# Optimization experiments

Hardware: AMD Instinct MI355X
Metric: run time of the kernel (lower is better)

## Reference

```python
import jax, jax.numpy as jnp
import numpy as np

VOCAB, EMB, HID = 50000, 256, 512
H = HID // 2            # per-direction LSTM hidden
NTAGS, START, STOP = 16, 14, 15
T = 2048                # sequence length
NEG = -10000.0


def setup_inputs() -> dict:
    key = jax.random.key(0)
    ks = jax.random.split(key, 13)
    s = 0.1  # param scale
    trans = jax.random.normal(ks[10], (NTAGS, NTAGS), jnp.float32)
    trans = trans.at[START, :].set(NEG).at[:, STOP].set(NEG)
    return {
        "sentence": jax.random.randint(ks[0], (T,), 0, VOCAB),
        "embed":  jax.random.normal(ks[1], (VOCAB, EMB), jnp.float32) * s,
        "w_ih_f": jax.random.normal(ks[2], (4 * H, EMB), jnp.float32) * s,
        "w_hh_f": jax.random.normal(ks[3], (4 * H, H), jnp.float32) * s,
        "b_f":    jax.random.normal(ks[4], (4 * H,), jnp.float32) * s,
        "w_ih_b": jax.random.normal(ks[5], (4 * H, EMB), jnp.float32) * s,
        "w_hh_b": jax.random.normal(ks[6], (4 * H, H), jnp.float32) * s,
        "b_b":    jax.random.normal(ks[7], (4 * H,), jnp.float32) * s,
        "w_out":  jax.random.normal(ks[8], (NTAGS, HID), jnp.float32) * s,
        "b_out":  jax.random.normal(ks[9], (NTAGS,), jnp.float32) * s,
        "transitions": trans,
        "h0": jax.random.normal(ks[11], (2, H), jnp.float32),
        "c0": jax.random.normal(ks[12], (2, H), jnp.float32),
    }


def _lstm_scan(xs, h0, c0, w_ih, w_hh, b):
    # xs: [T, EMB]; PyTorch gate order i, f, g, o
    def step(carry, x):
        h, c = carry
        g = x @ w_ih.T + h @ w_hh.T + b            # [4H]
        i, f, gg, o = jnp.split(g, 4)
        c = jax.nn.sigmoid(f) * c + jax.nn.sigmoid(i) * jnp.tanh(gg)
        h = jax.nn.sigmoid(o) * jnp.tanh(c)
        return (h, c), h
    _, hs = jax.lax.scan(step, (h0, c0), xs)
    return hs                                      # [T, H]


def _features(sentence, embed, w_ih_f, w_hh_f, b_f, w_ih_b, w_hh_b, b_b,
              w_out, b_out, h0, c0):
    xs = embed[sentence]                           # [T, EMB]
    hf = _lstm_scan(xs, h0[0], c0[0], w_ih_f, w_hh_f, b_f)
    hb = jnp.flip(_lstm_scan(jnp.flip(xs, 0), h0[1], c0[1], w_ih_b, w_hh_b, b_b), 0)
    lstm_out = jnp.concatenate([hf, hb], axis=-1)  # [T, HID]
    return lstm_out @ w_out.T + b_out              # [T, NTAGS]


def _viterbi(feats, transitions):
    init = jnp.full((NTAGS,), NEG, feats.dtype).at[START].set(0.0)

    def step(fv, feat):
        m = fv[None, :] + transitions              # [next, prev]
        return jnp.max(m, axis=1) + feat, jnp.argmax(m, axis=1)
    fv, bps = jax.lax.scan(step, init, feats)
    term = fv + transitions[STOP]
    best = jnp.argmax(term)
    score = term[best]

    def back(tag, bp):
        nt = bp[tag]
        return nt, nt
    _, ys = jax.lax.scan(back, best, jnp.flip(bps, 0))
    # [best, tag_{T-2}, ..., tag_0, START] -> drop START, reverse
    path = jnp.flip(jnp.concatenate([best[None], ys])[:-1])
    return score, path


def reference(sentence, embed, w_ih_f, w_hh_f, b_f, w_ih_b, w_hh_b, b_b,
              w_out, b_out, transitions, h0, c0):
    feats = _features(sentence, embed, w_ih_f, w_hh_f, b_f,
                      w_ih_b, w_hh_b, b_b, w_out, b_out, h0, c0)
    score, tag_seq = _viterbi(feats, transitions)
    return score, tag_seq
```

## Files before the change

### kernel.cpp

```cpp
#include <hip/hip_runtime.h>

typedef unsigned int u32;
typedef u32 u32x8 __attribute__((ext_vector_type(8)));

#define TT 2048
#define HD 256
#define G4 1024
#define NT 16
#define START_TAG 14
#define STOP_TAG 15
#define NEGV (-10000.0f)

__device__ __forceinline__ int sdot4e(u32 a, u32 b, int c) {
#if __has_builtin(__builtin_amdgcn_sdot4)
    return __builtin_amdgcn_sdot4((int)a, (int)b, c, false);
#else
    c += (int)(signed char)(a & 255) * (int)(signed char)(b & 255);
    c += (int)(signed char)((a >> 8) & 255) * (int)(signed char)((b >> 8) & 255);
    c += (int)(signed char)((a >> 16) & 255) * (int)(signed char)((b >> 16) & 255);
    c += (int)(signed char)(a >> 24) * (int)(signed char)(b >> 24);
    return c;
#endif
}
__device__ __forceinline__ float sigmf_(float x) { return 1.0f / (1.0f + __expf(-x)); }
__device__ __forceinline__ float tanhf_(float x) {
    float e = __expf(-2.0f * fabsf(x));
    return copysignf((1.0f - e) / (1.0f + e), x);
}

__global__ __launch_bounds__(256) void pack_q8(const float* whh_f, const float* whh_b,
                                               u32* wreg8, float* rowscale) {
    int lane = threadIdx.x & 63;
    int row = blockIdx.x * 4 + (threadIdx.x >> 6);
    int dir = row >> 10, r = row & 1023;
    const float* w = (dir ? whh_b : whh_f) + (size_t)r * HD + lane * 4;
    float4 v = *((const float4*)w);
    float m = fmaxf(fmaxf(fabsf(v.x), fabsf(v.y)), fmaxf(fabsf(v.z), fabsf(v.w)));
    for (int off = 1; off < 64; off <<= 1) m = fmaxf(m, __shfl_xor(m, off, 64));
    float invs = m > 0.f ? 127.f / m : 0.f;
    int q0 = (int)rintf(v.x * invs), q1 = (int)rintf(v.y * invs);
    int q2 = (int)rintf(v.z * invs), q3 = (int)rintf(v.w * invs);
    u32 pk = (u32)(q0 & 255) | ((u32)(q1 & 255) << 8) |
             ((u32)(q2 & 255) << 16) | ((u32)(q3 & 255) << 24);
    wreg8[((size_t)(dir * 1024 + r)) * 64 + lane] = pk;
    if (lane == 0) rowscale[dir * 1024 + r] = m * (1.0f / (127.f * 64.f));
}

__global__ __launch_bounds__(256) void input_gemm(const int* sent, const float* embed,
                                                  const float* wih_f, const float* b_f,
                                                  const float* wih_b, const float* b_b,
                                                  float* G) {
    __shared__ float X[16][HD];
    __shared__ int rows[16];
    int tid = threadIdx.x;
    int dir = blockIdx.z;
    int t0 = blockIdx.x * 16;
    if (tid < 16) {
        int tg = t0 + tid;
        rows[tid] = sent[dir ? (TT - 1 - tg) : tg];
    }
    __syncthreads();
    for (int i = 0; i < 16; i++) X[i][tid] = embed[(size_t)rows[i] * HD + tid];
    __syncthreads();
    int r = blockIdx.y * 256 + tid;
    const float* wrow = (dir ? wih_b : wih_f) + (size_t)r * HD;
    float acc[16];
#pragma unroll
    for (int i = 0; i < 16; i++) acc[i] = 0.0f;
    for (int kc = 0; kc < HD / 4; kc++) {
        float4 w4 = ((const float4*)wrow)[kc];
#pragma unroll
        for (int i = 0; i < 16; i++) {
            float4 x4 = *((const float4*)&X[i][kc * 4]);
            acc[i] += w4.x * x4.x + w4.y * x4.y + w4.z * x4.z + w4.w * x4.w;
        }
    }
    float bias = (dir ? b_b : b_f)[r];
    for (int i = 0; i < 16; i++)
        G[((size_t)dir * TT + t0 + i) * G4 + r] = acc[i] + bias;
}

#define DOTQ2(W0, W1, HB)                                                     \
    {                                                                         \
        uint4 pa = *((const uint4*)&h2q[(HB)]);                               \
        acc0 = sdot4e(W0[0], pa.x, acc0); acc1 = sdot4e(W1[0], pa.x, acc1);   \
        acc0 = sdot4e(W0[1], pa.y, acc0); acc1 = sdot4e(W1[1], pa.y, acc1);   \
        acc0 = sdot4e(W0[2], pa.z, acc0); acc1 = sdot4e(W1[2], pa.z, acc1);   \
        acc0 = sdot4e(W0[3], pa.w, acc0); acc1 = sdot4e(W1[3], pa.w, acc1);   \
        uint4 pb = *((const uint4*)&h2q[(HB) + 4]);                           \
        acc0 = sdot4e(W0[4], pb.x, acc0); acc1 = sdot4e(W1[4], pb.x, acc1);   \
        acc0 = sdot4e(W0[5], pb.y, acc0); acc1 = sdot4e(W1[5], pb.y, acc1);   \
        acc0 = sdot4e(W0[6], pb.z, acc0); acc1 = sdot4e(W1[6], pb.z, acc1);   \
        acc0 = sdot4e(W0[7], pb.w, acc0); acc1 = sdot4e(W1[7], pb.w, acc1);   \
    }

__global__ __launch_bounds__(512, 1)
void lstm_rec(const u32* wreg8, const float* rowscale,
              const float* G, const float* h0, const float* c0, float* H) {
    __shared__ float fo[2][256];
    __shared__ __align__(16) u32 h2q[64];
    int tid = threadIdx.x;
    int dir = blockIdx.x;
    const u32x8* p0 = (const u32x8*)(wreg8 + ((size_t)dir * 1024 + tid) * 64);
    const u32x8* p1 = (const u32x8*)(wreg8 + ((size_t)dir * 1024 + tid + 512) * 64);
    u32x8 wq00 = p0[0], wq01 = p0[1], wq02 = p0[2], wq03 = p0[3],
          wq04 = p0[4], wq05 = p0[5], wq06 = p0[6], wq07 = p0[7];
    u32x8 wq10 = p1[0], wq11 = p1[1], wq12 = p1[2], wq13 = p1[3],
          wq14 = p1[4], wq15 = p1[5], wq16 = p1[6], wq17 = p1[7];
    float cr0 = rowscale[dir * 1024 + tid];
    float cr1 = rowscale[dir * 1024 + tid + 512];
    float cst = 0.0f;
    if (tid < 256) {
        cst = c0[dir * HD + tid];
        float hv = h0[dir * HD + tid];
        hv = fminf(fmaxf(hv, -1.984375f), 1.984375f);
        ((signed char*)h2q)[tid] = (signed char)(int)rintf(hv * 64.f);
    }
    __syncthreads();
    const float* Gd = G + (size_t)dir * TT * G4;
    float* Hd = H + (size_t)dir * TT * HD;
    for (int t = 0; t < TT; t++) {
        float g0 = Gd[(size_t)t * G4 + tid];
        float g1 = Gd[(size_t)t * G4 + tid + 512];
        int acc0 = 0, acc1 = 0;
        DOTQ2(wq00, wq10, 0)  DOTQ2(wq01, wq11, 8)
        DOTQ2(wq02, wq12, 16) DOTQ2(wq03, wq13, 24)
        DOTQ2(wq04, wq14, 32) DOTQ2(wq05, wq15, 40)
        DOTQ2(wq06, wq16, 48) DOTQ2(wq07, wq17, 56)
        float e0 = (float)acc0 * cr0 + g0;
        float e1 = (float)acc1 * cr1 + g1;
        float x0, x1;
        if (tid >= 256) {
            fo[0][tid - 256] = sigmf_(e0);
            fo[1][tid - 256] = sigmf_(e1);
        } else {
            x0 = sigmf_(e0);
            x1 = tanhf_(e1);
        }
        __syncthreads();
        if (tid < 256) {
            float sf = fo[0][tid], so = fo[1][tid];
            cst = sf * cst + x0 * x1;
            float h = so * tanhf_(cst);
            Hd[(size_t)t * HD + tid] = h;
            ((signed char*)h2q)[tid] = (signed char)(int)rintf(h * 64.f);
        }
        __syncthreads();
    }
}

__global__ __launch_bounds__(256) void feats_kernel(const float* H, const float* w_out,
                                                    const float* b_out, float* feats) {
    int idx = blockIdx.x * blockDim.x + threadIdx.x;
    int t = idx >> 4, n = idx & 15;
    const float* hf = H + (size_t)t * HD;
    const float* hb = H + ((size_t)TT + (TT - 1 - t)) * HD;
    const float* w = w_out + (size_t)n * (2 * HD);
    float a = b_out[n];
    for (int k = 0; k < HD; k += 4) {
        float4 h4 = *((const float4*)&hf[k]);
        float4 w4 = *((const float4*)&w[k]);
        a += h4.x * w4.x + h4.y * w4.y + h4.z * w4.z + h4.w * w4.w;
    }
    for (int k = 0; k < HD; k += 4) {
        float4 h4 = *((const float4*)&hb[k]);
        float4 w4 = *((const float4*)&w[HD + k]);
        a += h4.x * w4.x + h4.y * w4.y + h4.z * w4.z + h4.w * w4.w;
    }
    feats[(size_t)t * NT + n] = a;
}

__global__ __launch_bounds__(64) void viterbi_kernel(const float* feats, const float* trans,
                                                     float* out) {
    __shared__ float fl[4096];
    __shared__ float fvs[NT];
    __shared__ unsigned char bps[TT][NT];
    int lane = threadIdx.x;
    int n = lane >> 2, pg = lane & 3;
    float4 tr4 = *((const float4*)&trans[n * NT + pg * 4]);
    float vft = (n == START_TAG) ? 0.0f : NEGV;
    for (int c = 0; c < TT / 256; c++) {
        float4 st[16];
        const float4* src = (const float4*)(feats + c * 4096);
#pragma unroll
        for (int i = 0; i < 16; i++) st[i] = src[i * 64 + lane];
#pragma unroll
        for (int i = 0; i < 16; i++) *((float4*)&fl[(i * 64 + lane) * 4]) = st[i];
        __syncthreads();
        for (int tt = 0; tt < 256; tt++) {
            int t = c * 256 + tt;
            float f0 = __shfl(vft, ((pg << 2) + 0) << 2, 64);
            float f1 = __shfl(vft, ((pg << 2) + 1) << 2, 64);
            float f2 = __shfl(vft, ((pg << 2) + 2) << 2, 64);
            float f3 = __shfl(vft, ((pg << 2) + 3) << 2, 64);
            float ft = fl[tt * 16 + n];
            float v = f0 + tr4.x; int bi = pg * 4 + 0;
            float v1 = f1 + tr4.y; if (v1 > v) { v = v1; bi = pg * 4 + 1; }
            float v2 = f2 + tr4.z; if (v2 > v) { v = v2; bi = pg * 4 + 2; }
            float v3 = f3 + tr4.w; if (v3 > v) { v = v3; bi = pg * 4 + 3; }
#pragma unroll
            for (int m = 1; m <= 2; m <<= 1) {
                float ov = __shfl_xor(v, m, 64);
                int ob = __shfl_xor(bi, m, 64);
                if (ov > v || (ov == v && ob < bi)) { v = ov; bi = ob; }
            }
            if (pg == 0) bps[t][n] = (unsigned char)bi;
            vft = v + ft;
        }
        __syncthreads();
    }
    if ((lane & 3) == 0) fvs[n] = vft;
    __syncthreads();
    if (lane == 0) {
        float best = -3.0e38f; int bt = 0;
        for (int p = 0; p < NT; p++) {
            float tv = fvs[p] + trans[STOP_TAG * NT + p];
            if (tv > best) { best = tv; bt = p; }
        }
        out[0] = best;
        int tag = bt;
        out[TT] = (float)tag;
        for (int t = TT - 2; t >= 0; t--) {
            tag = bps[t + 1][tag];
            out[1 + t] = (float)tag;
        }
    }
}

extern "C" void kernel_launch(void* const* d_in, const int* in_sizes, int n_in,
                              void* d_out, int out_size, void* d_ws, size_t ws_size,
                              hipStream_t stream) {
    const int* sent = (const int*)d_in[0];
    const float* embed = (const float*)d_in[1];
    const float* wih_f = (const float*)d_in[2];
    const float* whh_f = (const float*)d_in[3];
    const float* b_f = (const float*)d_in[4];
    const float* wih_b = (const float*)d_in[5];
    const float* whh_b = (const float*)d_in[6];
    const float* b_b = (const float*)d_in[7];
    const float* w_out = (const float*)d_in[8];
    const float* b_out = (const float*)d_in[9];
    const float* trans = (const float*)d_in[10];
    const float* h0 = (const float*)d_in[11];
    const float* c0 = (const float*)d_in[12];
    float* out = (float*)d_out;
    char* ws = (char*)d_ws;

    float* G = (float*)(ws);
    float* H = (float*)(ws + (size_t)16 * 1024 * 1024);
    float* feats = (float*)(ws + (size_t)20 * 1024 * 1024);
    u32* wreg8 = (u32*)(ws + (size_t)21 * 1024 * 1024);
    float* rowscale = (float*)(ws + (size_t)22 * 1024 * 1024);

    pack_q8<<<dim3(512), 256, 0, stream>>>(whh_f, whh_b, wreg8, rowscale);
    input_gemm<<<dim3(TT / 16, G4 / 256, 2), 256, 0, stream>>>(sent, embed, wih_f, b_f,
                                                               wih_b, b_b, G);
    lstm_rec<<<dim3(2), 512, 0, stream>>>(wreg8, rowscale, G, h0, c0, H);
    feats_kernel<<<dim3(TT * NT / 256), 256, 0, stream>>>(H, w_out, b_out, feats);
    viterbi_kernel<<<dim3(1), 64, 0, stream>>>(feats, trans, out);
}
```

Before: 2.610 ms.

## Drop one barrier per LSTM step and parallelize Viterbi backtrace

```diff
diff --git a/kernel.cpp b/kernel.cpp
--- a/kernel.cpp
+++ b/kernel.cpp
@@ -82,12 +82,12 @@
 
 #define DOTQ2(W0, W1, HB)                                                     \
     {                                                                         \
-        uint4 pa = *((const uint4*)&h2q[(HB)]);                               \
+        uint4 pa = *((const uint4*)&hbp[(HB)]);                               \
         acc0 = sdot4e(W0[0], pa.x, acc0); acc1 = sdot4e(W1[0], pa.x, acc1);   \
         acc0 = sdot4e(W0[1], pa.y, acc0); acc1 = sdot4e(W1[1], pa.y, acc1);   \
         acc0 = sdot4e(W0[2], pa.z, acc0); acc1 = sdot4e(W1[2], pa.z, acc1);   \
         acc0 = sdot4e(W0[3], pa.w, acc0); acc1 = sdot4e(W1[3], pa.w, acc1);   \
-        uint4 pb = *((const uint4*)&h2q[(HB) + 4]);                           \
+        uint4 pb = *((const uint4*)&hbp[(HB) + 4]);                           \
         acc0 = sdot4e(W0[4], pb.x, acc0); acc1 = sdot4e(W1[4], pb.x, acc1);   \
         acc0 = sdot4e(W0[5], pb.y, acc0); acc1 = sdot4e(W1[5], pb.y, acc1);   \
         acc0 = sdot4e(W0[6], pb.z, acc0); acc1 = sdot4e(W1[6], pb.z, acc1);   \
@@ -97,31 +97,42 @@
 __global__ __launch_bounds__(512, 1)
 void lstm_rec(const u32* wreg8, const float* rowscale,
               const float* G, const float* h0, const float* c0, float* H) {
-    __shared__ float fo[2][256];
-    __shared__ __align__(16) u32 h2q[64];
+    __shared__ __align__(16) u32 h2q[2][64];
     int tid = threadIdx.x;
+    int lane = tid & 63;
+    int wv = tid >> 6;
+    int lo = lane & 31;
+    int half = lane >> 5;
+    int e = wv * 32 + lo;
+    int row0 = half * 256 + e;
+    int row1 = row0 + 512;
     int dir = blockIdx.x;
-    const u32x8* p0 = (const u32x8*)(wreg8 + ((size_t)dir * 1024 + tid) * 64);
-    const u32x8* p1 = (const u32x8*)(wreg8 + ((size_t)dir * 1024 + tid + 512) * 64);
+    const u32x8* p0 = (const u32x8*)(wreg8 + ((size_t)dir * 1024 + row0) * 64);
+    const u32x8* p1 = (const u32x8*)(wreg8 + ((size_t)dir * 1024 + row1) * 64);
     u32x8 wq00 = p0[0], wq01 = p0[1], wq02 = p0[2], wq03 = p0[3],
           wq04 = p0[4], wq05 = p0[5], wq06 = p0[6], wq07 = p0[7];
     u32x8 wq10 = p1[0], wq11 = p1[1], wq12 = p1[2], wq13 = p1[3],
           wq14 = p1[4], wq15 = p1[5], wq16 = p1[6], wq17 = p1[7];
-    float cr0 = rowscale[dir * 1024 + tid];
-    float cr1 = rowscale[dir * 1024 + tid + 512];
-    float cst = 0.0f;
-    if (tid < 256) {
-        cst = c0[dir * HD + tid];
-        float hv = h0[dir * HD + tid];
+    float cr0 = rowscale[dir * 1024 + row0];
+    float cr1 = rowscale[dir * 1024 + row1];
+    float cst = (half == 0) ? c0[dir * HD + e] : 0.0f;
+    if (half == 0) {
+        float hv = h0[dir * HD + e];
         hv = fminf(fmaxf(hv, -1.984375f), 1.984375f);
-        ((signed char*)h2q)[tid] = (signed char)(int)rintf(hv * 64.f);
+        int hq = ((int)rintf(hv * 64.f)) & 255;
+        int b1 = __shfl_down(hq, 1, 64);
+        int b2 = __shfl_down(hq, 2, 64);
+        int b3 = __shfl_down(hq, 3, 64);
+        if ((lo & 3) == 0)
+            h2q[1][e >> 2] = (u32)hq | ((u32)b1 << 8) | ((u32)b2 << 16) | ((u32)b3 << 24);
     }
     __syncthreads();
     const float* Gd = G + (size_t)dir * TT * G4;
     float* Hd = H + (size_t)dir * TT * HD;
     for (int t = 0; t < TT; t++) {
-        float g0 = Gd[(size_t)t * G4 + tid];
-        float g1 = Gd[(size_t)t * G4 + tid + 512];
+        const u32* hbp = &h2q[(t + 1) & 1][0];
+        float g0 = Gd[(size_t)t * G4 + row0];
+        float g1 = Gd[(size_t)t * G4 + row1];
         int acc0 = 0, acc1 = 0;
         DOTQ2(wq00, wq10, 0)  DOTQ2(wq01, wq11, 8)
         DOTQ2(wq02, wq12, 16) DOTQ2(wq03, wq13, 24)
@@ -129,21 +140,23 @@
         DOTQ2(wq06, wq16, 48) DOTQ2(wq07, wq17, 56)
         float e0 = (float)acc0 * cr0 + g0;
         float e1 = (float)acc1 * cr1 + g1;
-        float x0, x1;
-        if (tid >= 256) {
-            fo[0][tid - 256] = sigmf_(e0);
-            fo[1][tid - 256] = sigmf_(e1);
-        } else {
-            x0 = sigmf_(e0);
-            x1 = tanhf_(e1);
-        }
-        __syncthreads();
-        if (tid < 256) {
-            float sf = fo[0][tid], so = fo[1][tid];
-            cst = sf * cst + x0 * x1;
-            float h = so * tanhf_(cst);
-            Hd[(size_t)t * HD + tid] = h;
-            ((signed char*)h2q)[tid] = (signed char)(int)rintf(h * 64.f);
+        float x0 = sigmf_(e0);
+        float xs = half ? e1 : (e1 + e1);
+        float s = sigmf_(xs);
+        float x1 = half ? s : (2.0f * s - 1.0f);
+        float y0 = __shfl_xor(x0, 32, 64);
+        float y1 = __shfl_xor(x1, 32, 64);
+        if (half == 0) {
+            cst = y0 * cst + x0 * x1;
+            float h = y1 * tanhf_(cst);
+            Hd[(size_t)t * HD + e] = h;
+            int hq = ((int)rintf(h * 64.f)) & 255;
+            int b1 = __shfl_down(hq, 1, 64);
+            int b2 = __shfl_down(hq, 2, 64);
+            int b3 = __shfl_down(hq, 3, 64);
+            if ((lo & 3) == 0)
+                h2q[t & 1][e >> 2] = (u32)hq | ((u32)b1 << 8) |
+                                     ((u32)b2 << 16) | ((u32)b3 << 24);
         }
         __syncthreads();
     }
@@ -170,59 +183,79 @@
     feats[(size_t)t * NT + n] = a;
 }
 
-__global__ __launch_bounds__(64) void viterbi_kernel(const float* feats, const float* trans,
-                                                     float* out) {
+__global__ __launch_bounds__(512) void viterbi_kernel(const float* feats, const float* trans,
+                                                      float* out) {
     __shared__ float fl[4096];
     __shared__ float fvs[NT];
     __shared__ unsigned char bps[TT][NT];
-    int lane = threadIdx.x;
+    __shared__ unsigned char Gtab[32 * 16];
+    __shared__ unsigned char Bnd[32];
+    __shared__ int bt_sh;
+    int tid = threadIdx.x;
+    int lane = tid & 63;
     int n = lane >> 2, pg = lane & 3;
     float4 tr4 = *((const float4*)&trans[n * NT + pg * 4]);
     float vft = (n == START_TAG) ? 0.0f : NEGV;
     for (int c = 0; c < TT / 256; c++) {
-        float4 st[16];
         const float4* src = (const float4*)(feats + c * 4096);
+        for (int i = tid; i < 1024; i += 512) ((float4*)fl)[i] = src[i];
+        __syncthreads();
+        if (tid < 64) {
+            for (int tt = 0; tt < 256; tt++) {
+                int t = c * 256 + tt;
+                float f0 = __shfl(vft, ((pg << 2) + 0) << 2, 64);
+                float f1 = __shfl(vft, ((pg << 2) + 1) << 2, 64);
+                float f2 = __shfl(vft, ((pg << 2) + 2) << 2, 64);
+                float f3 = __shfl(vft, ((pg << 2) + 3) << 2, 64);
+                float ft = fl[tt * 16 + n];
+                float v = f0 + tr4.x; int bi = pg * 4 + 0;
+                float v1 = f1 + tr4.y; if (v1 > v) { v = v1; bi = pg * 4 + 1; }
+                float v2 = f2 + tr4.z; if (v2 > v) { v = v2; bi = pg * 4 + 2; }
+                float v3 = f3 + tr4.w; if (v3 > v) { v = v3; bi = pg * 4 + 3; }
 #pragma unroll
-        for (int i = 0; i < 16; i++) st[i] = src[i * 64 + lane];
-#pragma unroll
-        for (int i = 0; i < 16; i++) *((float4*)&fl[(i * 64 + lane) * 4]) = st[i];
+                for (int m = 1; m <= 2; m <<= 1) {
+                    float ov = __shfl_xor(v, m, 64);
+                    int ob = __shfl_xor(bi, m, 64);
+                    if (ov > v || (ov == v && ob < bi)) { v = ov; bi = ob; }
+                }
+                if (pg == 0) bps[t][n] = (unsigned char)bi;
+                vft = v + ft;
+            }
+        }
         __syncthreads();
-        for (int tt = 0; tt < 256; tt++) {
-            int t = c * 256 + tt;
-            float f0 = __shfl(vft, ((pg << 2) + 0) << 2, 64);
-            float f1 = __shfl(vft, ((pg << 2) + 1) << 2, 64);
-            float f2 = __shfl(vft, ((pg << 2) + 2) << 2, 64);
-            float f3 = __shfl(vft, ((pg << 2) + 3) << 2, 64);
-            float ft = fl[tt * 16 + n];
-            float v = f0 + tr4.x; int bi = pg * 4 + 0;
-            float v1 = f1 + tr4.y; if (v1 > v) { v = v1; bi = pg * 4 + 1; }
-            float v2 = f2 + tr4.z; if (v2 > v) { v = v2; bi = pg * 4 + 2; }
-            float v3 = f3 + tr4.w; if (v3 > v) { v = v3; bi = pg * 4 + 3; }
-#pragma unroll
-            for (int m = 1; m <= 2; m <<= 1) {
-                float ov = __shfl_xor(v, m, 64);
-                int ob = __shfl_xor(bi, m, 64);
-                if (ov > v || (ov == v && ob < bi)) { v = ov; bi = ob; }
-            }
-            if (pg == 0) bps[t][n] = (unsigned char)bi;
-            vft = v + ft;
-        }
-        __syncthreads();
-    }
-    if ((lane & 3) == 0) fvs[n] = vft;
-    __syncthreads();
-    if (lane == 0) {
+    }
+    if (tid < 64 && (lane & 3) == 0) fvs[n] = vft;
+    __syncthreads();
+    if (tid == 0) {
         float best = -3.0e38f; int bt = 0;
         for (int p = 0; p < NT; p++) {
             float tv = fvs[p] + trans[STOP_TAG * NT + p];
             if (tv > best) { best = tv; bt = p; }
         }
         out[0] = best;
-        int tag = bt;
-        out[TT] = (float)tag;
-        for (int t = TT - 2; t >= 0; t--) {
-            tag = bps[t + 1][tag];
-            out[1 + t] = (float)tag;
+        bt_sh = bt;
+    }
+    __syncthreads();
+    if (tid < 496) {
+        int seg = 1 + (tid >> 4), tg = tid & 15;
+        int x = tg;
+        for (int k = 63; k >= 0; k--) x = bps[seg * 64 + k][x];
+        Gtab[seg * 16 + tg] = (unsigned char)x;
+    }
+    __syncthreads();
+    if (tid == 0) {
+        int x = bt_sh;
+        Bnd[31] = (unsigned char)x;
+        for (int s = 31; s >= 1; s--) { x = Gtab[s * 16 + x]; Bnd[s - 1] = (unsigned char)x; }
+    }
+    __syncthreads();
+    if (tid < 32) {
+        int s = tid;
+        int x = Bnd[s];
+        out[1 + s * 64 + 63] = (float)x;
+        for (int k = 63; k >= 1; k--) {
+            x = bps[s * 64 + k][x];
+            out[1 + s * 64 + k - 1] = (float)x;
         }
     }
 }
@@ -257,5 +290,5 @@
                                                                wih_b, b_b, G);
     lstm_rec<<<dim3(2), 512, 0, stream>>>(wreg8, rowscale, G, h0, c0, H);
     feats_kernel<<<dim3(TT * NT / 256), 256, 0, stream>>>(H, w_out, b_out, feats);
-    viterbi_kernel<<<dim3(1), 64, 0, stream>>>(feats, trans, out);
-}
+    viterbi_kernel<<<dim3(1), 512, 0, stream>>>(feats, trans, out);
+}
```

After: 2.690 ms. +3.1%, slower.

## Parallelize Viterbi via max-plus segment matrices and widen input GEMM per-thread rows

Applied to the files above, without the earlier changes.

```diff
diff --git a/kernel.cpp b/kernel.cpp
--- a/kernel.cpp
+++ b/kernel.cpp
@@ -62,22 +62,29 @@
     __syncthreads();
     for (int i = 0; i < 16; i++) X[i][tid] = embed[(size_t)rows[i] * HD + tid];
     __syncthreads();
-    int r = blockIdx.y * 256 + tid;
-    const float* wrow = (dir ? wih_b : wih_f) + (size_t)r * HD;
-    float acc[16];
-#pragma unroll
-    for (int i = 0; i < 16; i++) acc[i] = 0.0f;
+    int r = blockIdx.y * 512 + tid;
+    const float* base = dir ? wih_b : wih_f;
+    const float* wrowA = base + (size_t)r * HD;
+    const float* wrowB = base + (size_t)(r + 256) * HD;
+    float accA[16], accB[16];
+#pragma unroll
+    for (int i = 0; i < 16; i++) { accA[i] = 0.0f; accB[i] = 0.0f; }
     for (int kc = 0; kc < HD / 4; kc++) {
-        float4 w4 = ((const float4*)wrow)[kc];
+        float4 wa = ((const float4*)wrowA)[kc];
+        float4 wb = ((const float4*)wrowB)[kc];
 #pragma unroll
         for (int i = 0; i < 16; i++) {
             float4 x4 = *((const float4*)&X[i][kc * 4]);
-            acc[i] += w4.x * x4.x + w4.y * x4.y + w4.z * x4.z + w4.w * x4.w;
-        }
-    }
-    float bias = (dir ? b_b : b_f)[r];
-    for (int i = 0; i < 16; i++)
-        G[((size_t)dir * TT + t0 + i) * G4 + r] = acc[i] + bias;
+            accA[i] += wa.x * x4.x + wa.y * x4.y + wa.z * x4.z + wa.w * x4.w;
+            accB[i] += wb.x * x4.x + wb.y * x4.y + wb.z * x4.z + wb.w * x4.w;
+        }
+    }
+    const float* bb = dir ? b_b : b_f;
+    float biasA = bb[r], biasB = bb[r + 256];
+    for (int i = 0; i < 16; i++) {
+        G[((size_t)dir * TT + t0 + i) * G4 + r] = accA[i] + biasA;
+        G[((size_t)dir * TT + t0 + i) * G4 + r + 256] = accB[i] + biasB;
+    }
 }
 
 #define DOTQ2(W0, W1, HB)                                                     \
@@ -170,30 +177,86 @@
     feats[(size_t)t * NT + n] = a;
 }
 
-__global__ __launch_bounds__(64) void viterbi_kernel(const float* feats, const float* trans,
-                                                     float* out) {
-    __shared__ float fl[4096];
-    __shared__ float fvs[NT];
-    __shared__ unsigned char bps[TT][NT];
-    int lane = threadIdx.x;
+__global__ __launch_bounds__(1024) void vit_segmat(const float* feats, const float* trans,
+                                                   float* Mbuf) {
+    int tid = threadIdx.x;
+    int lane = tid & 63;
+    int col = tid >> 6;
+    int s = blockIdx.x;
     int n = lane >> 2, pg = lane & 3;
     float4 tr4 = *((const float4*)&trans[n * NT + pg * 4]);
-    float vft = (n == START_TAG) ? 0.0f : NEGV;
-    for (int c = 0; c < TT / 256; c++) {
-        float4 st[16];
-        const float4* src = (const float4*)(feats + c * 4096);
-#pragma unroll
-        for (int i = 0; i < 16; i++) st[i] = src[i * 64 + lane];
-#pragma unroll
-        for (int i = 0; i < 16; i++) *((float4*)&fl[(i * 64 + lane) * 4]) = st[i];
-        __syncthreads();
-        for (int tt = 0; tt < 256; tt++) {
-            int t = c * 256 + tt;
+    float vft = (n == col) ? 0.0f : NEGV;
+    const float* fseg = feats + s * 64 * NT;
+    float ftn = fseg[n];
+    for (int k = 0; k < 64; k++) {
+        float f0 = __shfl(vft, ((pg << 2) + 0) << 2, 64);
+        float f1 = __shfl(vft, ((pg << 2) + 1) << 2, 64);
+        float f2 = __shfl(vft, ((pg << 2) + 2) << 2, 64);
+        float f3 = __shfl(vft, ((pg << 2) + 3) << 2, 64);
+        float ft = ftn;
+        if (k + 1 < 64) ftn = fseg[(k + 1) * NT + n];
+        float v = fmaxf(fmaxf(f0 + tr4.x, f1 + tr4.y), fmaxf(f2 + tr4.z, f3 + tr4.w));
+#pragma unroll
+        for (int m = 1; m <= 2; m <<= 1) v = fmaxf(v, __shfl_xor(v, m, 64));
+        vft = v + ft;
+    }
+    if (pg == 0) Mbuf[(s * 16 + n) * 16 + col] = vft;
+}
+
+__global__ __launch_bounds__(1024) void vit_solve(const float* feats, const float* trans,
+                                                  const float* Mbuf, float* out) {
+    __shared__ float Msh[32 * 256];
+    __shared__ float Bnd[33][16];
+    __shared__ unsigned char bps[TT][NT];
+    __shared__ unsigned char Gtab[32 * 16];
+    __shared__ unsigned char BndT[32];
+    __shared__ int bt_sh;
+    int tid = threadIdx.x;
+    int lane = tid & 63;
+    int wv = tid >> 6;
+    int n = lane >> 2, pg = lane & 3;
+    for (int i = tid; i < 32 * 256 / 4; i += 1024)
+        ((float4*)Msh)[i] = ((const float4*)Mbuf)[i];
+    __syncthreads();
+    if (wv == 0) {
+        float vft = (n == START_TAG) ? 0.0f : NEGV;
+        if (pg == 0) Bnd[0][n] = vft;
+        for (int s = 0; s < 32; s++) {
+            float4 m4 = *((const float4*)&Msh[(s * 16 + n) * 16 + pg * 4]);
             float f0 = __shfl(vft, ((pg << 2) + 0) << 2, 64);
             float f1 = __shfl(vft, ((pg << 2) + 1) << 2, 64);
             float f2 = __shfl(vft, ((pg << 2) + 2) << 2, 64);
             float f3 = __shfl(vft, ((pg << 2) + 3) << 2, 64);
-            float ft = fl[tt * 16 + n];
+            float v = fmaxf(fmaxf(f0 + m4.x, f1 + m4.y), fmaxf(f2 + m4.z, f3 + m4.w));
+#pragma unroll
+            for (int m = 1; m <= 2; m <<= 1) v = fmaxf(v, __shfl_xor(v, m, 64));
+            vft = v;
+            if (pg == 0) Bnd[s + 1][n] = vft;
+        }
+        if (lane == 0) {
+            float best = -3.0e38f; int bt = 0;
+            for (int p = 0; p < NT; p++) {
+                float tv = Bnd[32][p] + trans[STOP_TAG * NT + p];
+                if (tv > best) { best = tv; bt = p; }
+            }
+            out[0] = best;
+            bt_sh = bt;
+        }
+    }
+    __syncthreads();
+    float4 tr4 = *((const float4*)&trans[n * NT + pg * 4]);
+    for (int rep = 0; rep < 2; rep++) {
+        int s = wv + rep * 16;
+        float vft = Bnd[s][n];
+        const float* fseg = feats + s * 64 * NT;
+        float ftn = fseg[n];
+        for (int k = 0; k < 64; k++) {
+            float f0 = __shfl(vft, ((pg << 2) + 0) << 2, 64);
+            float f1 = __shfl(vft, ((pg << 2) + 1) << 2, 64);
+            float f2 = __shfl(vft, ((pg << 2) + 2) << 2, 64);
+            float f3 = __shfl(vft, ((pg << 2) + 3) << 2, 64);
+            float ft = ftn;
+            if (k + 1 < 64) ftn = fseg[(k + 1) * NT + n];
             float v = f0 + tr4.x; int bi = pg * 4 + 0;
             float v1 = f1 + tr4.y; if (v1 > v) { v = v1; bi = pg * 4 + 1; }
             float v2 = f2 + tr4.z; if (v2 > v) { v = v2; bi = pg * 4 + 2; }
@@ -204,25 +267,31 @@
                 int ob = __shfl_xor(bi, m, 64);
                 if (ov > v || (ov == v && ob < bi)) { v = ov; bi = ob; }
             }
-            if (pg == 0) bps[t][n] = (unsigned char)bi;
+            if (pg == 0) bps[s * 64 + k][n] = (unsigned char)bi;
             vft = v + ft;
         }
-        __syncthreads();
-    }
-    if ((lane & 3) == 0) fvs[n] = vft;
-    __syncthreads();
-    if (lane == 0) {
-        float best = -3.0e38f; int bt = 0;
-        for (int p = 0; p < NT; p++) {
-            float tv = fvs[p] + trans[STOP_TAG * NT + p];
-            if (tv > best) { best = tv; bt = p; }
-        }
-        out[0] = best;
-        int tag = bt;
-        out[TT] = (float)tag;
-        for (int t = TT - 2; t >= 0; t--) {
-            tag = bps[t + 1][tag];
-            out[1 + t] = (float)tag;
+    }
+    __syncthreads();
+    if (tid < 496) {
+        int seg = 1 + (tid >> 4), tg = tid & 15;
+        int x = tg;
+        for (int k = 63; k >= 0; k--) x = bps[seg * 64 + k][x];
+        Gtab[seg * 16 + tg] = (unsigned char)x;
+    }
+    __syncthreads();
+    if (tid == 0) {
+        int x = bt_sh;
+        BndT[31] = (unsigned char)x;
+        for (int s = 31; s >= 1; s--) { x = Gtab[s * 16 + x]; BndT[s - 1] = (unsigned char)x; }
+    }
+    __syncthreads();
+    if (tid < 32) {
+        int s = tid;
+        int x = BndT[s];
+        out[1 + s * 64 + 63] = (float)x;
+        for (int k = 63; k >= 1; k--) {
+            x = bps[s * 64 + k][x];
+            out[1 + s * 64 + k - 1] = (float)x;
         }
     }
 }
@@ -251,11 +320,13 @@
     float* feats = (float*)(ws + (size_t)20 * 1024 * 1024);
     u32* wreg8 = (u32*)(ws + (size_t)21 * 1024 * 1024);
     float* rowscale = (float*)(ws + (size_t)22 * 1024 * 1024);
+    float* Mbuf = (float*)(ws + (size_t)22 * 1024 * 1024 + 64 * 1024);
 
     pack_q8<<<dim3(512), 256, 0, stream>>>(whh_f, whh_b, wreg8, rowscale);
-    input_gemm<<<dim3(TT / 16, G4 / 256, 2), 256, 0, stream>>>(sent, embed, wih_f, b_f,
-                                                               wih_b, b_b, G);
+    input_gemm<<<dim3(TT / 16, 2, 2), 256, 0, stream>>>(sent, embed, wih_f, b_f,
+                                                        wih_b, b_b, G);
     lstm_rec<<<dim3(2), 512, 0, stream>>>(wreg8, rowscale, G, h0, c0, H);
     feats_kernel<<<dim3(TT * NT / 256), 256, 0, stream>>>(H, w_out, b_out, feats);
-    viterbi_kernel<<<dim3(1), 64, 0, stream>>>(feats, trans, out);
-}
+    vit_segmat<<<dim3(32), 1024, 0, stream>>>(feats, trans, Mbuf);
+    vit_solve<<<dim3(1), 1024, 0, stream>>>(feats, trans, Mbuf, out);
+}
```

Result: faster. 2.105 ms (median of 2 runs) (-19.4%).
